# Performance work log

Measured on AMD Instinct MI355X. Metric: run time of the kernel, lower is better.

## Reference

```python
import jax, jax.numpy as jnp
import numpy as np
import math

U = 1024      # units
H = 16        # num_head
DH = U // H   # units_head
B = 2
Q = 1024      # query length
M = 1024      # memory length
KL = M + Q    # key length
R = KL + 1    # relative positions length (rel-shift needs k_len+1)
EPS = 1e-7    # K.epsilon()


def setup_inputs() -> dict:
    key = jax.random.key(0)
    ks = jax.random.split(key, 11)
    f32 = jnp.float32
    return {
        "inputs": jax.random.normal(ks[0], (B, Q, U), f32),
        "content": jax.random.normal(ks[1], (B, Q, U), f32),
        "memories": jax.random.normal(ks[2], (B, M, U), f32),
        "relatives": jax.random.normal(ks[3], (B, R, U), f32),
        "segment_mat": jax.random.uniform(ks[4], (B, Q, KL, 2), f32),
        "segment_embed": jax.random.normal(ks[5], (2, U), f32) * 0.02,
        "bias_context": jax.random.normal(ks[6], (U,), f32) * 0.02,
        "bias_relative": jax.random.normal(ks[7], (U,), f32) * 0.02,
        "bias_segment": jax.random.normal(ks[8], (U,), f32) * 0.02,
        "permutation": jax.random.uniform(ks[9], (B, Q, KL), f32),
        "kernel": jax.random.normal(ks[10], (U, 5 * U), f32) * 0.02,
    }


def _heads(x):
    # [B, L, U] -> [B, H, L, DH]
    b, l, _ = x.shape
    return x.reshape(b, l, H, DH).transpose(0, 2, 1, 3)


def _rel_shift(x, klen):
    # Transformer-XL relative shift via reshape trick. x: [B, H, Q, R]
    b, h, q, r = x.shape
    x = x.reshape(b, h, r, q)[:, :, 1:, :].reshape(b, h, q, r - 1)
    return x[:, :, :, :klen]


def reference(inputs, content, memories, relatives, segment_mat, segment_embed,
              bias_context, bias_relative, bias_segment, permutation, kernel):
    k_q = kernel[:, :U]
    k_kv = kernel[:, U:3 * U]
    k_r = kernel[:, 3 * U:4 * U]
    k_o = kernel[:, 4 * U:5 * U]

    full = jnp.concatenate([memories, content], axis=1)          # [B, KL, U]
    w_q = inputs @ k_q                                           # [B, Q, U]
    w_kv = full @ k_kv                                           # [B, KL, 2U]
    w_r = relatives @ k_r                                        # [B, R, U]

    w_k = _heads(w_kv[..., :U])                                  # [B, H, KL, DH]
    w_v = _heads(w_kv[..., U:])                                  # [B, H, KL, DH]

    # content term
    q_c = _heads(w_q + bias_context)                             # [B, H, Q, DH]
    a_context = jnp.einsum('bhqd,bhkd->bhqk', q_c, w_k)

    # relative-position term with rel-shift
    q_r = _heads(w_q + bias_relative)
    w_r_h = _heads(w_r)                                          # [B, H, R, DH]
    a_relative = _rel_shift(jnp.einsum('bhqd,bhrd->bhqr', q_r, w_r_h), KL)

    # segment term
    q_s = _heads(w_q + bias_segment)                             # [B, H, Q, DH]
    seg_e = segment_embed.T.reshape(H, DH, 2)                    # [H, DH, 2]
    qs_seg = jnp.einsum('bhqd,hds->bhqs', q_s, seg_e)            # [B, H, Q, 2]
    a_segment = jnp.einsum('bqks,bhqs->bhqk', segment_mat, qs_seg)

    att = (a_context + a_relative + a_segment) / math.sqrt(DH)   # [B, H, Q, KL]
    e = jnp.exp(att - jnp.max(att, axis=-1, keepdims=True))
    e = e * permutation[:, None, :, :]
    att = e / (jnp.sum(e, axis=-1, keepdims=True) + EPS)

    out = jnp.einsum('bhqk,bhkd->bhqd', att, w_v)                # [B, H, Q, DH]
    out = out.transpose(0, 2, 1, 3).reshape(inputs.shape[0], Q, U)
    return out @ k_o                                             # [B, Q, U]
```

## Files before the change

### kernel.cpp

```cpp
#include <hip/hip_runtime.h>

typedef __bf16 bf16;
typedef unsigned short u16;
typedef unsigned int u32;
typedef __attribute__((ext_vector_type(8))) __bf16 bf16x8;
typedef __attribute__((ext_vector_type(4))) __bf16 bf16x4;
typedef __attribute__((ext_vector_type(4))) float f32x4;
typedef __attribute__((ext_vector_type(8))) float f32x8;

#define SWZ(r, s) (((r) << 3) + ((s) ^ ((r) & 7)))
#define GSW(r, s) (((r) << 2) + ((s) ^ (((r) >> 1) & 3)))

__device__ __forceinline__ f32x4 mfma16(bf16x8 a, bf16x8 b, f32x4 c) {
  return __builtin_amdgcn_mfma_f32_16x16x32_bf16(a, b, c, 0, 0, 0);
}
__device__ __forceinline__ void gld16(const void* g, void* l) {
  __builtin_amdgcn_global_load_lds((const __attribute__((address_space(1))) void*)g,
                                   (__attribute__((address_space(3))) void*)l, 16, 0, 0);
}

__global__ __launch_bounds__(256) void prep_all(
    const float* __restrict__ inputs, const float* __restrict__ mem,
    const float* __restrict__ cont, const float* __restrict__ rel,
    const float* __restrict__ K, bf16* __restrict__ in_b,
    bf16* __restrict__ full_b, bf16* __restrict__ rel_b, bf16* __restrict__ KT) {
  __shared__ float t[64][68];
  const int bid = blockIdx.x, tid = threadIdx.x;
  if (bid < 1024) {
    size_t i = ((size_t)bid * 256 + tid) * 8;
    f32x8 v = *reinterpret_cast<const f32x8*>(inputs + i);
    *reinterpret_cast<bf16x8*>(in_b + i) = __builtin_convertvector(v, bf16x8);
  } else if (bid < 3072) {
    size_t i = ((size_t)(bid - 1024) * 256 + tid) * 8;
    int row = (int)(i >> 10), col = (int)(i & 1023);
    int b = row >> 11, r = row & 2047;
    const float* src = (r < 1024)
        ? (mem  + (((size_t)(b << 10) + r)          << 10) + col)
        : (cont + (((size_t)(b << 10) + (r - 1024)) << 10) + col);
    f32x8 v = *reinterpret_cast<const f32x8*>(src);
    *reinterpret_cast<bf16x8*>(full_b + i) = __builtin_convertvector(v, bf16x8);
  } else if (bid < 5121) {
    size_t i = ((size_t)(bid - 3072) * 256 + tid) * 8;
    f32x8 v = *reinterpret_cast<const f32x8*>(rel + i);
    *reinterpret_cast<bf16x8*>(rel_b + i) = __builtin_convertvector(v, bf16x8);
  } else {
    const int r = bid - 5121;
    const int n0 = (r % 80) << 6, k0 = (r / 80) << 6;
    for (int idx = tid; idx < 1024; idx += 256) {
      int rr = idx >> 4, c4 = (idx & 15) << 2;
      f32x4 v = *reinterpret_cast<const f32x4*>(K + (size_t)(k0 + rr) * 5120 + n0 + c4);
      t[rr][c4] = v.x; t[rr][c4 + 1] = v.y; t[rr][c4 + 2] = v.z; t[rr][c4 + 3] = v.w;
    }
    __syncthreads();
    for (int idx = tid; idx < 1024; idx += 256) {
      int rr = idx >> 4, c4 = (idx & 15) << 2;
      bf16x4 o = { (bf16)t[c4][rr], (bf16)t[c4 + 1][rr], (bf16)t[c4 + 2][rr], (bf16)t[c4 + 3][rr] };
      *reinterpret_cast<bf16x4*>(KT + (size_t)(n0 + rr) * 1024 + k0 + c4) = o;
    }
  }
}

template<int MT, int OUT_MODE, int KLEN, bool KWRAP>
__device__ __forceinline__ void gemm_body(
    const bf16* __restrict__ A, const bf16* __restrict__ BT,
    void* __restrict__ C0v, void* __restrict__ C1v,
    int m0, int n0, int Mrows, int splitN, bf16* As, bf16* Bs, int tid) {
  const int l = tid & 63, w = tid >> 6;
  const int wn = (w & 1) << 6;
  const int wm = (w >> 1) * (MT / 2);
  constexpr int MFR = MT / 32;
  const int lc = l & 15, l16 = l >> 4;
  f32x4 acc[MFR][4] = {};
  const int r0 = tid >> 2;
  const int sq = tid & 3;
  const int g0 = (sq ^ ((r0 >> 1) & 3)) << 3;

  for (int k0 = 0; k0 < KLEN; k0 += 32) {
    const int kk = KWRAP ? (k0 & 1023) : k0;
    __syncthreads();
    gld16(A  + (size_t)(m0 + r0) * KLEN + k0 + g0, &As[tid << 3]);
    gld16(BT + (size_t)(n0 + r0) * 1024 + kk + g0, &Bs[tid << 3]);
    if (MT == 128)
      gld16(A + (size_t)(m0 + r0 + 64) * KLEN + k0 + g0, &As[(tid + 256) << 3]);
    gld16(BT + (size_t)(n0 + r0 + 64) * 1024 + kk + g0, &Bs[(tid + 256) << 3]);
    __syncthreads();
    bf16x8 af[MFR], bfv[4];
#pragma unroll
    for (int m = 0; m < MFR; ++m)
      af[m] = *reinterpret_cast<const bf16x8*>(&As[GSW(wm + (m << 4) + lc, l16) << 3]);
#pragma unroll
    for (int n = 0; n < 4; ++n)
      bfv[n] = *reinterpret_cast<const bf16x8*>(&Bs[GSW(wn + (n << 4) + lc, l16) << 3]);
#pragma unroll
    for (int m = 0; m < MFR; ++m)
#pragma unroll
      for (int n = 0; n < 4; ++n)
        acc[m][n] = mfma16(af[m], bfv[n], acc[m][n]);
  }
#pragma unroll
  for (int m = 0; m < MFR; ++m) {
    const int rbase = m0 + wm + (m << 4) + (l16 << 2);
#pragma unroll
    for (int n = 0; n < 4; ++n) {
      const int col = n0 + wn + (n << 4) + lc;
      const int cc = (col < splitN) ? col : (col - splitN);
      void* Cv = (col < splitN) ? C0v : C1v;
#pragma unroll
      for (int r = 0; r < 4; ++r) {
        const int row = rbase + r;
        if (row < Mrows) {
          const float v = acc[m][n][r];
          const size_t off = ((size_t)row << 10) + cc;
          if (OUT_MODE == 1) ((bf16*)Cv)[off] = (bf16)v;
          else               ((float*)Cv)[off] = v;
        }
      }
    }
  }
}

__global__ __launch_bounds__(256) void proj_fused(
    const bf16* __restrict__ in_b, const bf16* __restrict__ full_b,
    const bf16* __restrict__ rel_b, const bf16* __restrict__ kT,
    bf16* __restrict__ w_q, bf16* __restrict__ w_k, bf16* __restrict__ w_v,
    bf16* __restrict__ w_rh) {
  __shared__ bf16 As[4096];
  __shared__ bf16 Bs[4096];
  const int bid = blockIdx.x, tid = threadIdx.x;
  if (bid < 256) {
    gemm_body<64, 1, 1024, false>(in_b, kT, w_q, w_q,
                                  (bid >> 3) << 6, (bid & 7) << 7, 2048, 1 << 30, As, Bs, tid);
  } else if (bid < 768) {
    const int r = bid - 256;
    gemm_body<128, 1, 1024, false>(full_b, kT + (1 << 20), w_k, w_v,
                                   (r >> 4) << 7, (r & 15) << 7, 4096, 1024, As, Bs, tid);
  } else {
    const int r = bid - 768;
    gemm_body<64, 1, 1024, false>(rel_b, kT + 3 * (1 << 20), w_rh, w_rh,
                                  (r >> 3) << 6, (r & 7) << 7, 4098, 1 << 30, As, Bs, tid);
  }
}

__global__ __launch_bounds__(256) void out_proj(
    const bf16* __restrict__ a_cat, const bf16* __restrict__ kTo,
    float* __restrict__ out) {
  __shared__ bf16 As[4096];
  __shared__ bf16 Bs[4096];
  const int bid = blockIdx.x, tid = threadIdx.x;
  gemm_body<64, 0, 2048, true>(a_cat, kTo, out, out,
                               (bid >> 3) << 6, (bid & 7) << 7, 2048, 1 << 30, As, Bs, tid);
}

__global__ __launch_bounds__(256) void mid_prep(
    const float* __restrict__ seg_mat, bf16* __restrict__ seg_b,
    const bf16* __restrict__ w_q, const float* __restrict__ bias_s,
    const float* __restrict__ seg_embed, float* __restrict__ qs) {
  const int bid = blockIdx.x, tid = threadIdx.x;
  if (bid < 4096) {
    size_t i = ((size_t)bid * 256 + tid) * 8;
    f32x8 v = *reinterpret_cast<const f32x8*>(seg_mat + i);
    *reinterpret_cast<bf16x8*>(seg_b + i) = __builtin_convertvector(v, bf16x8);
  } else {
    int idx = (bid - 4096) * 256 + tid;
    int q = idx & 1023, h = (idx >> 10) & 15, b = idx >> 14;
    const bf16* wp = w_q + (((size_t)(b << 10) + q) << 10) + (h << 6);
    const float* bp = bias_s + (h << 6);
    const float* e0 = seg_embed + (h << 6);
    const float* e1 = seg_embed + 1024 + (h << 6);
    float s0 = 0.f, s1 = 0.f;
#pragma unroll 8
    for (int d = 0; d < 64; ++d) {
      float v = (float)wp[d] + bp[d];
      s0 = fmaf(v, e0[d], s0);
      s1 = fmaf(v, e1[d], s1);
    }
    qs[((size_t)idx << 1) + 0] = s0;
    qs[((size_t)idx << 1) + 1] = s1;
  }
}

#define OFFA 7
#define OFFB 0

__global__ __launch_bounds__(256) void attn_mfma(
    const bf16* __restrict__ w_q, const bf16* __restrict__ w_k,
    const bf16* __restrict__ w_v, const bf16* __restrict__ w_rh,
    const float* __restrict__ qs_seg, const bf16* __restrict__ seg_b,
    const float* __restrict__ perm, const float* __restrict__ bias_c,
    const float* __restrict__ bias_r, bf16* __restrict__ a_cat) {
  const int id = blockIdx.x;
  const int h  = (id >> 3) & 15;
  const int cg = (id & 7) | ((id >> 7) << 3);
  const int qt = cg & 15, b = cg >> 4;
  const int qi0 = qt << 6;
  const int tid = threadIdx.x;
  const int w = tid >> 6, l = tid & 63;
  const int lc = l & 15, l16 = l >> 4;
  const int w16 = w << 4;
  const int myq = w16 + lc;

  __shared__ bf16 kt[2][32 * 64];
  __shared__ u16  vt[2][64 * 40];
  __shared__ bf16 wbc[128 * 64];
  __shared__ bf16 wb2[96 * 64];
  __shared__ u16  pl[64 * 40];
  __shared__ float ART[4 * 960];
  __shared__ float facw[64], lroww[64];

  auto stageK = [&](int buf, int kj) {
    int r = tid >> 3, s = tid & 7;
    gld16(w_k + ((size_t)((b << 11) + kj + r) << 10) + (h << 6) + ((s ^ (r & 7)) << 3),
          &kt[buf][tid << 3]);
  };
  auto stageWB = [&](int L0, int nrows, int OFF) {
    for (int base = 0; base < nrows; base += 32) {
      int r = (tid >> 3) + base, s = tid & 7;
      int L = L0 + r;
      int slot = (L + OFF) & 127;
      int grow = L > 2048 ? 2048 : L;
      gld16(w_rh + ((size_t)(b * 2049 + grow) << 10) + (h << 6) + ((s ^ (slot & 7)) << 3),
            &wbc[((slot << 3) | s) << 3]);
    }
  };
  auto stageWB2 = [&]() {
    for (int base = 0; base < 96; base += 32) {
      int r = (tid >> 3) + base, s = tid & 7;
      gld16(w_rh + ((size_t)(b * 2049 + r) << 10) + (h << 6) + ((s ^ (r & 7)) << 3),
            &wb2[((r << 3) | s) << 3]);
    }
  };
  const int kv2 = (tid & 15) << 1, d4 = ((tid >> 4) & 15) << 2, kw = tid & 15;
  auto loadV = [&](int kj, uint2& ra, uint2& rb) {
    const u16* vp = (const u16*)w_v + ((size_t)((b << 11) + kj + kv2) << 10) + (h << 6) + d4;
    ra = *reinterpret_cast<const uint2*>(vp);
    rb = *reinterpret_cast<const uint2*>(vp + 1024);
  };
  auto writeV = [&](int buf, uint2 ra, uint2 rb) {
    u32* vt32 = reinterpret_cast<u32*>(&vt[buf][0]);
    vt32[(d4 + 0) * 20 + kw] = (ra.x & 0xffffu) | (rb.x << 16);
    vt32[(d4 + 1) * 20 + kw] = (ra.x >> 16) | (rb.x & 0xffff0000u);
    vt32[(d4 + 2) * 20 + kw] = (ra.y & 0xffffu) | (rb.y << 16);
    vt32[(d4 + 3) * 20 + kw] = (ra.y >> 16) | (rb.y & 0xffff0000u);
  };
  const size_t qrowg = (size_t)((b << 10) + qi0 + myq);
  auto loadSP = [&](int kj, bf16x8& sA, bf16x8& sB, f32x4& pA, f32x4& pB) {
    const bf16* sp = seg_b + (qrowg * 2048 + kj + (l16 << 2)) * 2;
    sA = *reinterpret_cast<const bf16x8*>(sp);
    sB = *reinterpret_cast<const bf16x8*>(sp + 32);
    const float* pp = perm + qrowg * 2048 + kj + (l16 << 2);
    pA = *reinterpret_cast<const f32x4*>(pp);
    pB = *reinterpret_cast<const f32x4*>(pp + 16);
  };

  stageK(0, 0);
  stageWB(961 - qi0, 96, OFFA);
  uint2 ra0, rb0;
  loadV(0, ra0, rb0);
  bf16x8 segA_c, segB_c, segA_n = {}, segB_n = {};
  f32x4 pmA_c, pmB_c, pmA_n = {}, pmB_n = {};
  loadSP(0, segA_c, segB_c, pmA_c, pmB_c);

  const int dlo = l16 << 3;
  bf16x8 qcf0, qcf1, qrf0, qrf1, qrg0, qrg1;
  {
    const bf16* qb  = w_q + ((qrowg) << 10) + (h << 6);
    const int rq1 = (qi0 + myq + 1 > 1023) ? 1023 : qi0 + myq + 1;
    const bf16* qb1 = w_q + (((size_t)(b << 10) + rq1) << 10) + (h << 6);
    f32x8 bc0 = *reinterpret_cast<const f32x8*>(bias_c + (h << 6) + dlo);
    f32x8 bc1 = *reinterpret_cast<const f32x8*>(bias_c + (h << 6) + 32 + dlo);
    f32x8 br0 = *reinterpret_cast<const f32x8*>(bias_r + (h << 6) + dlo);
    f32x8 br1 = *reinterpret_cast<const f32x8*>(bias_r + (h << 6) + 32 + dlo);
    bf16x8 q0 = *reinterpret_cast<const bf16x8*>(qb + dlo);
    bf16x8 q1 = *reinterpret_cast<const bf16x8*>(qb + 32 + dlo);
    bf16x8 p0 = *reinterpret_cast<const bf16x8*>(qb1 + dlo);
    bf16x8 p1 = *reinterpret_cast<const bf16x8*>(qb1 + 32 + dlo);
    qcf0 = __builtin_convertvector(__builtin_convertvector(q0, f32x8) + bc0, bf16x8);
    qcf1 = __builtin_convertvector(__builtin_convertvector(q1, f32x8) + bc1, bf16x8);
    qrf0 = __builtin_convertvector(__builtin_convertvector(q0, f32x8) + br0, bf16x8);
    qrf1 = __builtin_convertvector(__builtin_convertvector(q1, f32x8) + br1, bf16x8);
    qrg0 = __builtin_convertvector(__builtin_convertvector(p0, f32x8) + br0, bf16x8);
    qrg1 = __builtin_convertvector(__builtin_convertvector(p1, f32x8) + br1, bf16x8);
  }
  const float* qp = qs_seg + ((((size_t)((b << 4) + h) << 10) + qi0 + myq) << 1);
  const float qs0 = qp[0], qs1 = qp[1];

  writeV(0, ra0, rb0);
  __syncthreads();

  float mrow = -1e30f, lrow = 0.f;
  f32x4 o[4] = {};
  const float SCL = 0.125f * 1.44269504f;
  int cur = 0;
  uint2 ra_n = {}, rb_n = {};

  for (int t = 0; t < 64; ++t) {
    const int kj = t << 5;
    const int rel0 = kj - qi0;
    const bool strad = (rel0 == 1024) | (rel0 == 1056);
    const bool mainB = (rel0 >= 1088);
    const int nxt = cur ^ 1;

    if (t < 63) {
      const int kjn = kj + 32, rel0n = rel0 + 32;
      stageK(nxt, kjn);
      if (rel0n == 1024) stageWB2();
      if (rel0n == 1120)      stageWB(32, 96, OFFB);
      else if (rel0n != 1088) {
        if (rel0n <= 1056) stageWB(rel0n + 1025, 32, OFFA);
        else               stageWB(rel0n - 1024, 32, OFFB);
      }
      loadV(kjn, ra_n, rb_n);
      loadSP(kjn, segA_n, segB_n, pmA_n, pmB_n);
    }

    f32x4 s0 = {0.f, 0.f, 0.f, 0.f}, s1 = {0.f, 0.f, 0.f, 0.f};
    {
      const bf16* ktc = kt[cur];
      bf16x8 a0 = *reinterpret_cast<const bf16x8*>(&ktc[SWZ(lc, l16) << 3]);
      bf16x8 a1 = *reinterpret_cast<const bf16x8*>(&ktc[SWZ(lc, l16 + 4) << 3]);
      bf16x8 a2 = *reinterpret_cast<const bf16x8*>(&ktc[SWZ(16 + lc, l16) << 3]);
      bf16x8 a3 = *reinterpret_cast<const bf16x8*>(&ktc[SWZ(16 + lc, l16 + 4) << 3]);
      __builtin_amdgcn_s_setprio(1);
      s0 = mfma16(a0, qcf0, s0); s0 = mfma16(a1, qcf1, s0);
      s1 = mfma16(a2, qcf0, s1); s1 = mfma16(a3, qcf1, s1);
      __builtin_amdgcn_s_setprio(0);
    }

    float relv[8];
    {
      const bf16x8 ar0 = mainB ? qrg0 : qrf0;
      const bf16x8 ar1 = mainB ? qrg1 : qrf1;
      const bool useWb2 = (rel0 == 1088);
      int sbase;
      if (!mainB)       sbase = (rel0 + 1016 - w16) & 127;
      else if (useWb2)  sbase = 48 - w16;
      else              sbase = (rel0 - 1040 - w16) & 127;
      const bf16* wbp = useWb2 ? wb2 : wbc;
#pragma unroll
      for (int bg = 0; bg < 3; ++bg) {
        int prow = sbase + (bg << 4) + lc;
        if (!useWb2) prow &= 127;
        bf16x8 w0 = *reinterpret_cast<const bf16x8*>(&wbp[SWZ(prow, l16) << 3]);
        bf16x8 w1 = *reinterpret_cast<const bf16x8*>(&wbp[SWZ(prow, l16 + 4) << 3]);
        f32x4 a_ = {0.f, 0.f, 0.f, 0.f};
        __builtin_amdgcn_s_setprio(1);
        a_ = mfma16(ar0, w0, a_); a_ = mfma16(ar1, w1, a_);
        __builtin_amdgcn_s_setprio(0);
        *reinterpret_cast<f32x4*>(&ART[w * 960 + ((bg << 4) + lc) * 20 + (l16 << 2)]) = a_;
      }
#pragma unroll
      for (int jj = 0; jj < 4; ++jj) {
        relv[jj]     = ART[w * 960 + (15 + (l16 << 2) + jj - lc) * 20 + lc];
        relv[4 + jj] = ART[w * 960 + (31 + (l16 << 2) + jj - lc) * 20 + lc];
      }
      if (strad) {
#pragma unroll
        for (int bg = 0; bg < 3; ++bg) {
          int srow = rel0 - 1040 - w16 + (bg << 4) + lc;
          srow = srow < 0 ? 0 : (srow > 95 ? 95 : srow);
          bf16x8 w0 = *reinterpret_cast<const bf16x8*>(&wb2[SWZ(srow, l16) << 3]);
          bf16x8 w1 = *reinterpret_cast<const bf16x8*>(&wb2[SWZ(srow, l16 + 4) << 3]);
          f32x4 a_ = {0.f, 0.f, 0.f, 0.f};
          a_ = mfma16(qrg0, w0, a_); a_ = mfma16(qrg1, w1, a_);
          *reinterpret_cast<f32x4*>(&ART[w * 960 + ((bg << 4) + lc) * 20 + (l16 << 2)]) = a_;
        }
#pragma unroll
        for (int jj = 0; jj < 4; ++jj) {
          const int jA = (l16 << 2) + jj, jB = 16 + jA;
          float rbA = ART[w * 960 + (15 + jA - lc) * 20 + lc];
          float rbB = ART[w * 960 + (15 + jB - lc) * 20 + lc];
          if (rel0 + jA - myq >= 1025) relv[jj] = rbA;
          if (rel0 + jB - myq >= 1025) relv[4 + jj] = rbB;
        }
      }
    }

    {
      f32x8 sgA = __builtin_convertvector(segA_c, f32x8);
      f32x8 sgB = __builtin_convertvector(segB_c, f32x8);
      float sv[8];
#pragma unroll
      for (int jj = 0; jj < 4; ++jj) {
        sv[jj]     = (s0[jj] + relv[jj]     + sgA[2 * jj] * qs0 + sgA[2 * jj + 1] * qs1) * SCL;
        sv[4 + jj] = (s1[jj] + relv[4 + jj] + sgB[2 * jj] * qs0 + sgB[2 * jj + 1] * qs1) * SCL;
      }
      float tm = sv[0];
#pragma unroll
      for (int jj = 1; jj < 8; ++jj) tm = fmaxf(tm, sv[jj]);
      tm = fmaxf(tm, __shfl_xor(tm, 16));
      tm = fmaxf(tm, __shfl_xor(tm, 32));
      const float mn2 = fmaxf(mrow, tm);
      const float facr = exp2f(mrow - mn2);
      float e[8], rs = 0.f;
#pragma unroll
      for (int jj = 0; jj < 4; ++jj) {
        e[jj]     = exp2f(sv[jj] - mn2) * pmA_c[jj];
        e[4 + jj] = exp2f(sv[4 + jj] - mn2) * pmB_c[jj];
        rs += e[jj] + e[4 + jj];
      }
      rs += __shfl_xor(rs, 16);
      rs += __shfl_xor(rs, 32);
      mrow = mn2;
      lrow = lrow * facr + rs;
      bf16x4 pa, pb;
#pragma unroll
      for (int jj = 0; jj < 4; ++jj) { pa[jj] = (bf16)e[jj]; pb[jj] = (bf16)e[4 + jj]; }
      *reinterpret_cast<bf16x4*>(&pl[myq * 40 + (l16 << 2)]) = pa;
      *reinterpret_cast<bf16x4*>(&pl[myq * 40 + 16 + (l16 << 2)]) = pb;
      if (l16 == 0) facw[myq] = facr;
    }

    {
      float fr[4];
#pragma unroll
      for (int r = 0; r < 4; ++r) fr[r] = facw[w16 + (l16 << 2) + r];
#pragma unroll
      for (int n = 0; n < 4; ++n)
#pragma unroll
        for (int r = 0; r < 4; ++r) o[n][r] *= fr[r];
      bf16x8 ap = *reinterpret_cast<const bf16x8*>(&pl[(w16 + lc) * 40 + (l16 << 3)]);
      bf16x8 bv0 = *reinterpret_cast<const bf16x8*>(&vt[cur][(lc) * 40 + (l16 << 3)]);
      bf16x8 bv1 = *reinterpret_cast<const bf16x8*>(&vt[cur][(16 + lc) * 40 + (l16 << 3)]);
      bf16x8 bv2 = *reinterpret_cast<const bf16x8*>(&vt[cur][(32 + lc) * 40 + (l16 << 3)]);
      bf16x8 bv3 = *reinterpret_cast<const bf16x8*>(&vt[cur][(48 + lc) * 40 + (l16 << 3)]);
      __builtin_amdgcn_s_setprio(1);
      o[0] = mfma16(ap, bv0, o[0]);
      o[1] = mfma16(ap, bv1, o[1]);
      o[2] = mfma16(ap, bv2, o[2]);
      o[3] = mfma16(ap, bv3, o[3]);
      __builtin_amdgcn_s_setprio(0);
    }

    if (t < 63) {
      writeV(nxt, ra_n, rb_n);
      segA_c = segA_n; segB_c = segB_n; pmA_c = pmA_n; pmB_c = pmB_n;
    }
    __syncthreads();
    cur = nxt;
  }

  if (l16 == 0) lroww[myq] = lrow;
  {
    float inv[4];
#pragma unroll
    for (int r = 0; r < 4; ++r)
      inv[r] = 1.f / (lroww[w16 + (l16 << 2) + r] + 1e-7f);
#pragma unroll
    for (int n = 0; n < 4; ++n) {
#pragma unroll
      for (int r = 0; r < 4; ++r) {
        const int row = qi0 + w16 + (l16 << 2) + r;
        const float v = o[n][r] * inv[r];
        const bf16 hi = (bf16)v;
        const float lof = v - (float)hi;
        const size_t off = (((size_t)(b << 10) + row) << 11) + (h << 6) + (n << 4) + lc;
        a_cat[off] = hi;
        a_cat[off + 1024] = (bf16)lof;
      }
    }
  }
}

extern "C" void kernel_launch(void* const* d_in, const int* in_sizes, int n_in,
                              void* d_out, int out_size, void* d_ws, size_t ws_size,
                              hipStream_t stream) {
  (void)in_sizes; (void)n_in; (void)out_size; (void)ws_size;
  const float* inputs    = (const float*)d_in[0];
  const float* content   = (const float*)d_in[1];
  const float* memories  = (const float*)d_in[2];
  const float* relatives = (const float*)d_in[3];
  const float* seg_mat   = (const float*)d_in[4];
  const float* seg_embed = (const float*)d_in[5];
  const float* bias_c    = (const float*)d_in[6];
  const float* bias_r    = (const float*)d_in[7];
  const float* bias_s    = (const float*)d_in[8];
  const float* perm      = (const float*)d_in[9];
  const float* kern      = (const float*)d_in[10];
  float* out = (float*)d_out;

  char* ws = (char*)d_ws;
  bf16*  in_b   = (bf16*)(ws);
  bf16*  full_b = (bf16*)(ws + 4194304);
  bf16*  rel_b  = (bf16*)(ws + 12582912);
  bf16*  kT     = (bf16*)(ws + 21233664);
  bf16*  w_q    = (bf16*)(ws + 31719424);
  bf16*  w_k    = (bf16*)(ws + 35913728);
  bf16*  w_v    = (bf16*)(ws + 44302336);
  bf16*  w_rh   = (bf16*)(ws + 52690944);
  float* qs     = (float*)(ws + 65277952);
  bf16*  seg_b  = (bf16*)(ws);
  bf16*  a_cat  = (bf16*)(ws + 21233664);
  bf16*  kTo    = (bf16*)(ws + 29622272);

  dim3 blk(256);
  prep_all<<<6401, blk, 0, stream>>>(inputs, memories, content, relatives, kern,
                                     in_b, full_b, rel_b, kT);
  proj_fused<<<1288, blk, 0, stream>>>(in_b, full_b, rel_b, kT, w_q, w_k, w_v, w_rh);
  mid_prep<<<4224, blk, 0, stream>>>(seg_mat, seg_b, w_q, bias_s, seg_embed, qs);
  attn_mfma<<<512, blk, 0, stream>>>(w_q, w_k, w_v, w_rh, qs, seg_b, perm,
                                     bias_c, bias_r, a_cat);
  out_proj<<<256, blk, 0, stream>>>(a_cat, kTo, out);
}
```

Baseline: 269.3 us.

## Split attention key range across two blocks and merge partial softmax results

The attention kernel now splits each (batch, head, query-tile) over two key halves, launching 1024 blocks instead of 512. Each block writes unnormalized outputs plus row max and sum to workspace chunks, and a new merge kernel combines them into a_cat. This raises parallelism on the many-CU GPU. Shared memory is also trimmed by reusing a pool, with the relative-score staging stored in bf16 for the upper half. Per-row scale factors now travel by wave shuffles instead of LDS, and the setprio hints are removed. The cost is an extra kernel launch, a workspace round trip, and lower precision on the upper half's relative scores.

```diff
diff --git a/kernel.cpp b/kernel.cpp
--- a/kernel.cpp
+++ b/kernel.cpp
@@ -18,6 +18,15 @@
   __builtin_amdgcn_global_load_lds((const __attribute__((address_space(1))) void*)g,
                                    (__attribute__((address_space(3))) void*)l, 16, 0, 0);
 }
+
+__device__ __forceinline__ float* chunk_ptr(char* ws, int c) {
+  size_t off;
+  if (c < 17)      off = 16777216u + (size_t)c * 262144u;
+  else if (c < 49) off = 21233664u + (size_t)(c - 17) * 262144u;
+  else             off = 61083648u + (size_t)(c - 49) * 262144u;
+  return (float*)(ws + off);
+}
+#define ML_OFF 65540096u
 
 __global__ __launch_bounds__(256) void prep_all(
     const float* __restrict__ inputs, const float* __restrict__ mem,
@@ -179,33 +188,34 @@
   }
 }
 
-#define OFFA 7
-#define OFFB 0
-
 __global__ __launch_bounds__(256) void attn_mfma(
     const bf16* __restrict__ w_q, const bf16* __restrict__ w_k,
     const bf16* __restrict__ w_v, const bf16* __restrict__ w_rh,
     const float* __restrict__ qs_seg, const bf16* __restrict__ seg_b,
     const float* __restrict__ perm, const float* __restrict__ bias_c,
-    const float* __restrict__ bias_r, bf16* __restrict__ a_cat) {
+    const float* __restrict__ bias_r, char* __restrict__ ws) {
   const int id = blockIdx.x;
-  const int h  = (id >> 3) & 15;
-  const int cg = (id & 7) | ((id >> 7) << 3);
-  const int qt = cg & 15, b = cg >> 4;
+  const int h    = id & 15;
+  const int qt   = (id >> 4) & 15;
+  const int half = (id >> 8) & 1;
+  const int b    = (id >> 9) & 1;
+  const bool up  = (half == 1);
   const int qi0 = qt << 6;
+  const int kj0 = half << 10;
   const int tid = threadIdx.x;
   const int w = tid >> 6, l = tid & 63;
   const int lc = l & 15, l16 = l >> 4;
   const int w16 = w << 4;
   const int myq = w16 + lc;
 
-  __shared__ bf16 kt[2][32 * 64];
-  __shared__ u16  vt[2][64 * 40];
-  __shared__ bf16 wbc[128 * 64];
-  __shared__ bf16 wb2[96 * 64];
-  __shared__ u16  pl[64 * 40];
-  __shared__ float ART[4 * 960];
-  __shared__ float facw[64], lroww[64];
+  __shared__ bf16 kt[2][2048];
+  __shared__ u16  vt[2][2560];
+  __shared__ bf16 wbc[8192];
+  __shared__ __align__(16) char upool[15872];
+  float* artL = (float*)upool;
+  bf16*  wb2v = (bf16*)upool;
+  u16*   artU = (u16*)(upool + 8192);
+  u16*   plw  = up ? (u16*)(upool + 8192 + w * 1920) : (u16*)(upool + w * 3840);
 
   auto stageK = [&](int buf, int kj) {
     int r = tid >> 3, s = tid & 7;
@@ -223,10 +233,10 @@
     }
   };
   auto stageWB2 = [&]() {
-    for (int base = 0; base < 96; base += 32) {
+    for (int base = 0; base < 64; base += 32) {
       int r = (tid >> 3) + base, s = tid & 7;
       gld16(w_rh + ((size_t)(b * 2049 + r) << 10) + (h << 6) + ((s ^ (r & 7)) << 3),
-            &wb2[((r << 3) | s) << 3]);
+            &wb2v[((r << 3) | s) << 3]);
     }
   };
   const int kv2 = (tid & 15) << 1, d4 = ((tid >> 4) & 15) << 2, kw = tid & 15;
@@ -251,14 +261,25 @@
     pA = *reinterpret_cast<const f32x4*>(pp);
     pB = *reinterpret_cast<const f32x4*>(pp + 16);
   };
-
-  stageK(0, 0);
-  stageWB(961 - qi0, 96, OFFA);
+  auto artWr = [&](int bandcol, f32x4 a_) {
+    int idx = w * 960 + bandcol * 20 + (l16 << 2);
+    if (up) *reinterpret_cast<bf16x4*>(&artU[idx]) = __builtin_convertvector(a_, bf16x4);
+    else    *reinterpret_cast<f32x4*>(&artL[idx]) = a_;
+  };
+  auto artRd = [&](int col) -> float {
+    int idx = w * 960 + col * 20 + lc;
+    return up ? (float)(reinterpret_cast<const bf16*>(artU)[idx]) : artL[idx];
+  };
+
+  const int rel0f = kj0 - qi0;
+  stageK(0, kj0);
+  stageWB(rel0f + 961, 96, 7);
+  if (up && rel0f == 1024) stageWB2();
   uint2 ra0, rb0;
-  loadV(0, ra0, rb0);
+  loadV(kj0, ra0, rb0);
   bf16x8 segA_c, segB_c, segA_n = {}, segB_n = {};
   f32x4 pmA_c, pmB_c, pmA_n = {}, pmB_n = {};
-  loadSP(0, segA_c, segB_c, pmA_c, pmB_c);
+  loadSP(kj0, segA_c, segB_c, pmA_c, pmB_c);
 
   const int dlo = l16 << 3;
   bf16x8 qcf0, qcf1, qrf0, qrf1, qrg0, qrg1;
@@ -293,21 +314,25 @@
   int cur = 0;
   uint2 ra_n = {}, rb_n = {};
 
-  for (int t = 0; t < 64; ++t) {
-    const int kj = t << 5;
+  for (int t = 0; t < 32; ++t) {
+    const int kj = kj0 + (t << 5);
     const int rel0 = kj - qi0;
-    const bool strad = (rel0 == 1024) | (rel0 == 1056);
-    const bool mainB = (rel0 >= 1088);
+    const bool strad = up && ((rel0 == 1024) | (rel0 == 1056));
+    const bool mainB = up && (rel0 >= 1088);
+    const bool spec1088 = up && (rel0 == 1088);
     const int nxt = cur ^ 1;
 
-    if (t < 63) {
+    if (t < 31) {
       const int kjn = kj + 32, rel0n = rel0 + 32;
       stageK(nxt, kjn);
-      if (rel0n == 1024) stageWB2();
-      if (rel0n == 1120)      stageWB(32, 96, OFFB);
-      else if (rel0n != 1088) {
-        if (rel0n <= 1056) stageWB(rel0n + 1025, 32, OFFA);
-        else               stageWB(rel0n - 1024, 32, OFFB);
+      if (up) {
+        if (rel0n == 1024) stageWB2();
+        if (rel0n <= 1056)       stageWB(rel0n + 1025, 32, 7);
+        else if (rel0n == 1088)  stageWB(64, 32, 8);
+        else if (rel0n == 1120) { stageWB(32, 32, 8); stageWB(96, 32, 8); }
+        else                     stageWB(rel0n - 1024, 32, 8);
+      } else {
+        stageWB(rel0n + 1025, 32, 7);
       }
       loadV(kjn, ra_n, rb_n);
       loadSP(kjn, segA_n, segB_n, pmA_n, pmB_n);
@@ -320,61 +345,65 @@
       bf16x8 a1 = *reinterpret_cast<const bf16x8*>(&ktc[SWZ(lc, l16 + 4) << 3]);
       bf16x8 a2 = *reinterpret_cast<const bf16x8*>(&ktc[SWZ(16 + lc, l16) << 3]);
       bf16x8 a3 = *reinterpret_cast<const bf16x8*>(&ktc[SWZ(16 + lc, l16 + 4) << 3]);
-      __builtin_amdgcn_s_setprio(1);
       s0 = mfma16(a0, qcf0, s0); s0 = mfma16(a1, qcf1, s0);
       s1 = mfma16(a2, qcf0, s1); s1 = mfma16(a3, qcf1, s1);
-      __builtin_amdgcn_s_setprio(0);
     }
 
     float relv[8];
     {
       const bf16x8 ar0 = mainB ? qrg0 : qrf0;
       const bf16x8 ar1 = mainB ? qrg1 : qrf1;
-      const bool useWb2 = (rel0 == 1088);
       int sbase;
-      if (!mainB)       sbase = (rel0 + 1016 - w16) & 127;
-      else if (useWb2)  sbase = 48 - w16;
-      else              sbase = (rel0 - 1040 - w16) & 127;
-      const bf16* wbp = useWb2 ? wb2 : wbc;
+      if (!mainB) sbase = (rel0 + 1016 - w16) & 127;
+      else        sbase = (rel0 - 1032 - w16) & 127;
 #pragma unroll
       for (int bg = 0; bg < 3; ++bg) {
-        int prow = sbase + (bg << 4) + lc;
-        if (!useWb2) prow &= 127;
-        bf16x8 w0 = *reinterpret_cast<const bf16x8*>(&wbp[SWZ(prow, l16) << 3]);
-        bf16x8 w1 = *reinterpret_cast<const bf16x8*>(&wbp[SWZ(prow, l16 + 4) << 3]);
+        bf16x8 w0, w1;
+        if (spec1088) {
+          int Lr = 48 - w16 + (bg << 4) + lc;
+          const bf16* p0 = (Lr < 64) ? &wb2v[SWZ(Lr, l16) << 3]
+                                     : &wbc[SWZ((Lr + 8) & 127, l16) << 3];
+          const bf16* p1 = (Lr < 64) ? &wb2v[SWZ(Lr, l16 + 4) << 3]
+                                     : &wbc[SWZ((Lr + 8) & 127, l16 + 4) << 3];
+          w0 = *reinterpret_cast<const bf16x8*>(p0);
+          w1 = *reinterpret_cast<const bf16x8*>(p1);
+        } else {
+          int prow = (sbase + (bg << 4) + lc) & 127;
+          w0 = *reinterpret_cast<const bf16x8*>(&wbc[SWZ(prow, l16) << 3]);
+          w1 = *reinterpret_cast<const bf16x8*>(&wbc[SWZ(prow, l16 + 4) << 3]);
+        }
         f32x4 a_ = {0.f, 0.f, 0.f, 0.f};
-        __builtin_amdgcn_s_setprio(1);
         a_ = mfma16(ar0, w0, a_); a_ = mfma16(ar1, w1, a_);
-        __builtin_amdgcn_s_setprio(0);
-        *reinterpret_cast<f32x4*>(&ART[w * 960 + ((bg << 4) + lc) * 20 + (l16 << 2)]) = a_;
+        artWr((bg << 4) + lc, a_);
       }
 #pragma unroll
       for (int jj = 0; jj < 4; ++jj) {
-        relv[jj]     = ART[w * 960 + (15 + (l16 << 2) + jj - lc) * 20 + lc];
-        relv[4 + jj] = ART[w * 960 + (31 + (l16 << 2) + jj - lc) * 20 + lc];
+        relv[jj]     = artRd(15 + (l16 << 2) + jj - lc);
+        relv[4 + jj] = artRd(31 + (l16 << 2) + jj - lc);
       }
       if (strad) {
 #pragma unroll
         for (int bg = 0; bg < 3; ++bg) {
           int srow = rel0 - 1040 - w16 + (bg << 4) + lc;
-          srow = srow < 0 ? 0 : (srow > 95 ? 95 : srow);
-          bf16x8 w0 = *reinterpret_cast<const bf16x8*>(&wb2[SWZ(srow, l16) << 3]);
-          bf16x8 w1 = *reinterpret_cast<const bf16x8*>(&wb2[SWZ(srow, l16 + 4) << 3]);
+          srow = srow < 0 ? 0 : (srow > 63 ? 63 : srow);
+          bf16x8 w0 = *reinterpret_cast<const bf16x8*>(&wb2v[SWZ(srow, l16) << 3]);
+          bf16x8 w1 = *reinterpret_cast<const bf16x8*>(&wb2v[SWZ(srow, l16 + 4) << 3]);
           f32x4 a_ = {0.f, 0.f, 0.f, 0.f};
           a_ = mfma16(qrg0, w0, a_); a_ = mfma16(qrg1, w1, a_);
-          *reinterpret_cast<f32x4*>(&ART[w * 960 + ((bg << 4) + lc) * 20 + (l16 << 2)]) = a_;
+          artWr((bg << 4) + lc, a_);
         }
 #pragma unroll
         for (int jj = 0; jj < 4; ++jj) {
           const int jA = (l16 << 2) + jj, jB = 16 + jA;
-          float rbA = ART[w * 960 + (15 + jA - lc) * 20 + lc];
-          float rbB = ART[w * 960 + (15 + jB - lc) * 20 + lc];
+          float rbA = artRd(15 + jA - lc);
+          float rbB = artRd(15 + jB - lc);
           if (rel0 + jA - myq >= 1025) relv[jj] = rbA;
           if (rel0 + jB - myq >= 1025) relv[4 + jj] = rbB;
         }
       }
     }
 
+    float facr;
     {
       f32x8 sgA = __builtin_convertvector(segA_c, f32x8);
       f32x8 sgB = __builtin_convertvector(segB_c, f32x8);
@@ -390,7 +419,7 @@
       tm = fmaxf(tm, __shfl_xor(tm, 16));
       tm = fmaxf(tm, __shfl_xor(tm, 32));
       const float mn2 = fmaxf(mrow, tm);
-      const float facr = exp2f(mrow - mn2);
+      facr = exp2f(mrow - mn2);
       float e[8], rs = 0.f;
 #pragma unroll
       for (int jj = 0; jj < 4; ++jj) {
@@ -405,33 +434,32 @@
       bf16x4 pa, pb;
 #pragma unroll
       for (int jj = 0; jj < 4; ++jj) { pa[jj] = (bf16)e[jj]; pb[jj] = (bf16)e[4 + jj]; }
-      *reinterpret_cast<bf16x4*>(&pl[myq * 40 + (l16 << 2)]) = pa;
-      *reinterpret_cast<bf16x4*>(&pl[myq * 40 + 16 + (l16 << 2)]) = pb;
-      if (l16 == 0) facw[myq] = facr;
+      *reinterpret_cast<bf16x4*>(&plw[lc * 40 + (l16 << 2)]) = pa;
+      *reinterpret_cast<bf16x4*>(&plw[lc * 40 + 16 + (l16 << 2)]) = pb;
     }
 
     {
-      float fr[4];
-#pragma unroll
-      for (int r = 0; r < 4; ++r) fr[r] = facw[w16 + (l16 << 2) + r];
-#pragma unroll
-      for (int n = 0; n < 4; ++n)
-#pragma unroll
-        for (int r = 0; r < 4; ++r) o[n][r] *= fr[r];
-      bf16x8 ap = *reinterpret_cast<const bf16x8*>(&pl[(w16 + lc) * 40 + (l16 << 3)]);
+      const int r4 = l16 << 2;
+      float fr0 = __shfl(facr, r4 + 0);
+      float fr1 = __shfl(facr, r4 + 1);
+      float fr2 = __shfl(facr, r4 + 2);
+      float fr3 = __shfl(facr, r4 + 3);
+#pragma unroll
+      for (int n = 0; n < 4; ++n) {
+        o[n][0] *= fr0; o[n][1] *= fr1; o[n][2] *= fr2; o[n][3] *= fr3;
+      }
+      bf16x8 ap = *reinterpret_cast<const bf16x8*>(&plw[lc * 40 + (l16 << 3)]);
       bf16x8 bv0 = *reinterpret_cast<const bf16x8*>(&vt[cur][(lc) * 40 + (l16 << 3)]);
       bf16x8 bv1 = *reinterpret_cast<const bf16x8*>(&vt[cur][(16 + lc) * 40 + (l16 << 3)]);
       bf16x8 bv2 = *reinterpret_cast<const bf16x8*>(&vt[cur][(32 + lc) * 40 + (l16 << 3)]);
       bf16x8 bv3 = *reinterpret_cast<const bf16x8*>(&vt[cur][(48 + lc) * 40 + (l16 << 3)]);
-      __builtin_amdgcn_s_setprio(1);
       o[0] = mfma16(ap, bv0, o[0]);
       o[1] = mfma16(ap, bv1, o[1]);
       o[2] = mfma16(ap, bv2, o[2]);
       o[3] = mfma16(ap, bv3, o[3]);
-      __builtin_amdgcn_s_setprio(0);
-    }
-
-    if (t < 63) {
+    }
+
+    if (t < 31) {
       writeV(nxt, ra_n, rb_n);
       segA_c = segA_n; segB_c = segB_n; pmA_c = pmA_n; pmB_c = pmB_n;
     }
@@ -439,26 +467,61 @@
     cur = nxt;
   }
 
-  if (l16 == 0) lroww[myq] = lrow;
   {
-    float inv[4];
-#pragma unroll
-    for (int r = 0; r < 4; ++r)
-      inv[r] = 1.f / (lroww[w16 + (l16 << 2) + r] + 1e-7f);
+    const int c = ((((b << 4) + h) << 1) + half);
+    float* ob = chunk_ptr(ws, c);
 #pragma unroll
     for (int n = 0; n < 4; ++n) {
 #pragma unroll
       for (int r = 0; r < 4; ++r) {
         const int row = qi0 + w16 + (l16 << 2) + r;
-        const float v = o[n][r] * inv[r];
-        const bf16 hi = (bf16)v;
-        const float lof = v - (float)hi;
-        const size_t off = (((size_t)(b << 10) + row) << 11) + (h << 6) + (n << 4) + lc;
-        a_cat[off] = hi;
-        a_cat[off + 1024] = (bf16)lof;
-      }
-    }
-  }
+        ob[row * 64 + (n << 4) + lc] = o[n][r];
+      }
+    }
+    if (l16 == 0) {
+      float* ml = (float*)(ws + ML_OFF);
+      ml[c * 2048 + qi0 + myq] = mrow;
+      ml[c * 2048 + 1024 + qi0 + myq] = lrow;
+    }
+  }
+}
+
+__global__ __launch_bounds__(256) void merge_attn(char* __restrict__ ws,
+                                                  bf16* __restrict__ a_cat) {
+  const int gid = blockIdx.x * 256 + threadIdx.x;
+  const int r = gid >> 2;
+  const int dq = (gid & 3) << 4;
+  const int b = r >> 14, h = (r >> 10) & 15, q = r & 1023;
+  const int c0 = (((b << 4) + h) << 1);
+  const float* o1 = chunk_ptr(ws, c0)     + q * 64 + dq;
+  const float* o2 = chunk_ptr(ws, c0 + 1) + q * 64 + dq;
+  const float* ml = (const float*)(ws + ML_OFF);
+  const float m1 = ml[c0 * 2048 + q],        l1 = ml[c0 * 2048 + 1024 + q];
+  const float m2 = ml[(c0 + 1) * 2048 + q],  l2 = ml[(c0 + 1) * 2048 + 1024 + q];
+  const float m = fmaxf(m1, m2);
+  float a1 = exp2f(m1 - m), a2 = exp2f(m2 - m);
+  const float inv = 1.f / (l1 * a1 + l2 * a2 + 1e-7f);
+  a1 *= inv; a2 *= inv;
+  bf16x8 hi0, hi1, lo0, lo1;
+#pragma unroll
+  for (int j4 = 0; j4 < 4; ++j4) {
+    f32x4 v1 = *reinterpret_cast<const f32x4*>(o1 + (j4 << 2));
+    f32x4 v2 = *reinterpret_cast<const f32x4*>(o2 + (j4 << 2));
+#pragma unroll
+    for (int jj = 0; jj < 4; ++jj) {
+      const float v = v1[jj] * a1 + v2[jj] * a2;
+      const bf16 hi = (bf16)v;
+      const float lo = v - (float)hi;
+      const int j = (j4 << 2) + jj;
+      if (j < 8) { hi0[j] = hi; lo0[j] = (bf16)lo; }
+      else       { hi1[j - 8] = hi; lo1[j - 8] = (bf16)lo; }
+    }
+  }
+  const size_t off = ((size_t)((b << 10) + q)) * 2048 + (h << 6) + dq;
+  *reinterpret_cast<bf16x8*>(a_cat + off) = hi0;
+  *reinterpret_cast<bf16x8*>(a_cat + off + 8) = hi1;
+  *reinterpret_cast<bf16x8*>(a_cat + off + 1024) = lo0;
+  *reinterpret_cast<bf16x8*>(a_cat + off + 1032) = lo1;
 }
 
 extern "C" void kernel_launch(void* const* d_in, const int* in_sizes, int n_in,
@@ -489,7 +552,7 @@
   bf16*  w_rh   = (bf16*)(ws + 52690944);
   float* qs     = (float*)(ws + 65277952);
   bf16*  seg_b  = (bf16*)(ws);
-  bf16*  a_cat  = (bf16*)(ws + 21233664);
+  bf16*  a_cat  = (bf16*)(ws);
   bf16*  kTo    = (bf16*)(ws + 29622272);
 
   dim3 blk(256);
@@ -497,7 +560,8 @@
                                      in_b, full_b, rel_b, kT);
   proj_fused<<<1288, blk, 0, stream>>>(in_b, full_b, rel_b, kT, w_q, w_k, w_v, w_rh);
   mid_prep<<<4224, blk, 0, stream>>>(seg_mat, seg_b, w_q, bias_s, seg_embed, qs);
-  attn_mfma<<<512, blk, 0, stream>>>(w_q, w_k, w_v, w_rh, qs, seg_b, perm,
-                                     bias_c, bias_r, a_cat);
+  attn_mfma<<<1024, blk, 0, stream>>>(w_q, w_k, w_v, w_rh, qs, seg_b, perm,
+                                      bias_c, bias_r, ws);
+  merge_attn<<<512, blk, 0, stream>>>(ws, a_cat);
   out_proj<<<256, blk, 0, stream>>>(a_cat, kTo, out);
 }
```

Measured after the change: 316.8 us. 17.6% more time.

## Shrink attention LDS footprint, fold softmax scale into Q, add lazy rescaling

Applied to the files above, without the earlier changes.

Reduces shared memory in the attention kernel. The relative-score scratch now holds bf16 instead of fp32 and is reused as the P staging buffer, the wb2 buffer shrinks from 96 to 64 rows, and the facw/lroww arrays are replaced by wave shuffles. The softmax scale is folded into the Q fragments and segment coefficients, removing a per-element multiply. A lazy online-softmax rescale skips the max update and the output rescale unless a row's max grows by more than 8 (log2 units). The s_setprio hints are dropped. The goal is higher occupancy and less ALU work, at the cost of bf16 rounding of the relative logits and more complex staging logic for wbc and wb2v.

```diff
diff --git a/kernel.cpp b/kernel.cpp
--- a/kernel.cpp
+++ b/kernel.cpp
@@ -179,9 +179,6 @@
   }
 }
 
-#define OFFA 7
-#define OFFB 0
-
 __global__ __launch_bounds__(256) void attn_mfma(
     const bf16* __restrict__ w_q, const bf16* __restrict__ w_k,
     const bf16* __restrict__ w_v, const bf16* __restrict__ w_rh,
@@ -199,13 +196,12 @@
   const int w16 = w << 4;
   const int myq = w16 + lc;
 
-  __shared__ bf16 kt[2][32 * 64];
-  __shared__ u16  vt[2][64 * 40];
-  __shared__ bf16 wbc[128 * 64];
-  __shared__ bf16 wb2[96 * 64];
-  __shared__ u16  pl[64 * 40];
-  __shared__ float ART[4 * 960];
-  __shared__ float facw[64], lroww[64];
+  __shared__ bf16 kt[2][2048];
+  __shared__ u16  vt[2][2560];
+  __shared__ bf16 wbc[8192];
+  __shared__ bf16 wb2v[4096];
+  __shared__ u16  artp[3840];
+  u16* artw = &artp[w * 960];
 
   auto stageK = [&](int buf, int kj) {
     int r = tid >> 3, s = tid & 7;
@@ -223,10 +219,10 @@
     }
   };
   auto stageWB2 = [&]() {
-    for (int base = 0; base < 96; base += 32) {
+    for (int base = 0; base < 64; base += 32) {
       int r = (tid >> 3) + base, s = tid & 7;
       gld16(w_rh + ((size_t)(b * 2049 + r) << 10) + (h << 6) + ((s ^ (r & 7)) << 3),
-            &wb2[((r << 3) | s) << 3]);
+            &wb2v[((r << 3) | s) << 3]);
     }
   };
   const int kv2 = (tid & 15) << 1, d4 = ((tid >> 4) & 15) << 2, kw = tid & 15;
@@ -251,15 +247,23 @@
     pA = *reinterpret_cast<const f32x4*>(pp);
     pB = *reinterpret_cast<const f32x4*>(pp + 16);
   };
+  auto artWr = [&](int bandcol, f32x4 a_) {
+    *reinterpret_cast<bf16x4*>(&artw[bandcol * 20 + (l16 << 2)]) =
+        __builtin_convertvector(a_, bf16x4);
+  };
+  auto artRd = [&](int col) -> float {
+    return (float)(reinterpret_cast<const bf16*>(artw)[col * 20 + lc]);
+  };
 
   stageK(0, 0);
-  stageWB(961 - qi0, 96, OFFA);
+  stageWB(961 - qi0, 96, 7);
   uint2 ra0, rb0;
   loadV(0, ra0, rb0);
   bf16x8 segA_c, segB_c, segA_n = {}, segB_n = {};
   f32x4 pmA_c, pmB_c, pmA_n = {}, pmB_n = {};
   loadSP(0, segA_c, segB_c, pmA_c, pmB_c);
 
+  const float SCLF = 0.125f * 1.44269504f;
   const int dlo = l16 << 3;
   bf16x8 qcf0, qcf1, qrf0, qrf1, qrg0, qrg1;
   {
@@ -274,22 +278,21 @@
     bf16x8 q1 = *reinterpret_cast<const bf16x8*>(qb + 32 + dlo);
     bf16x8 p0 = *reinterpret_cast<const bf16x8*>(qb1 + dlo);
     bf16x8 p1 = *reinterpret_cast<const bf16x8*>(qb1 + 32 + dlo);
-    qcf0 = __builtin_convertvector(__builtin_convertvector(q0, f32x8) + bc0, bf16x8);
-    qcf1 = __builtin_convertvector(__builtin_convertvector(q1, f32x8) + bc1, bf16x8);
-    qrf0 = __builtin_convertvector(__builtin_convertvector(q0, f32x8) + br0, bf16x8);
-    qrf1 = __builtin_convertvector(__builtin_convertvector(q1, f32x8) + br1, bf16x8);
-    qrg0 = __builtin_convertvector(__builtin_convertvector(p0, f32x8) + br0, bf16x8);
-    qrg1 = __builtin_convertvector(__builtin_convertvector(p1, f32x8) + br1, bf16x8);
+    qcf0 = __builtin_convertvector((__builtin_convertvector(q0, f32x8) + bc0) * SCLF, bf16x8);
+    qcf1 = __builtin_convertvector((__builtin_convertvector(q1, f32x8) + bc1) * SCLF, bf16x8);
+    qrf0 = __builtin_convertvector((__builtin_convertvector(q0, f32x8) + br0) * SCLF, bf16x8);
+    qrf1 = __builtin_convertvector((__builtin_convertvector(q1, f32x8) + br1) * SCLF, bf16x8);
+    qrg0 = __builtin_convertvector((__builtin_convertvector(p0, f32x8) + br0) * SCLF, bf16x8);
+    qrg1 = __builtin_convertvector((__builtin_convertvector(p1, f32x8) + br1) * SCLF, bf16x8);
   }
   const float* qp = qs_seg + ((((size_t)((b << 4) + h) << 10) + qi0 + myq) << 1);
-  const float qs0 = qp[0], qs1 = qp[1];
+  const float qs0 = qp[0] * SCLF, qs1 = qp[1] * SCLF;
 
   writeV(0, ra0, rb0);
   __syncthreads();
 
   float mrow = -1e30f, lrow = 0.f;
   f32x4 o[4] = {};
-  const float SCL = 0.125f * 1.44269504f;
   int cur = 0;
   uint2 ra_n = {}, rb_n = {};
 
@@ -298,17 +301,17 @@
     const int rel0 = kj - qi0;
     const bool strad = (rel0 == 1024) | (rel0 == 1056);
     const bool mainB = (rel0 >= 1088);
+    const bool spec1088 = (rel0 == 1088);
     const int nxt = cur ^ 1;
 
     if (t < 63) {
       const int kjn = kj + 32, rel0n = rel0 + 32;
       stageK(nxt, kjn);
       if (rel0n == 1024) stageWB2();
-      if (rel0n == 1120)      stageWB(32, 96, OFFB);
-      else if (rel0n != 1088) {
-        if (rel0n <= 1056) stageWB(rel0n + 1025, 32, OFFA);
-        else               stageWB(rel0n - 1024, 32, OFFB);
-      }
+      if (rel0n <= 1056)       stageWB(rel0n + 1025, 32, 7);
+      else if (rel0n == 1088)  stageWB(64, 32, 8);
+      else if (rel0n == 1120) { stageWB(32, 32, 8); stageWB(96, 32, 8); }
+      else                     stageWB(rel0n - 1024, 32, 8);
       loadV(kjn, ra_n, rb_n);
       loadSP(kjn, segA_n, segB_n, pmA_n, pmB_n);
     }
@@ -320,115 +323,126 @@
       bf16x8 a1 = *reinterpret_cast<const bf16x8*>(&ktc[SWZ(lc, l16 + 4) << 3]);
       bf16x8 a2 = *reinterpret_cast<const bf16x8*>(&ktc[SWZ(16 + lc, l16) << 3]);
       bf16x8 a3 = *reinterpret_cast<const bf16x8*>(&ktc[SWZ(16 + lc, l16 + 4) << 3]);
-      __builtin_amdgcn_s_setprio(1);
       s0 = mfma16(a0, qcf0, s0); s0 = mfma16(a1, qcf1, s0);
       s1 = mfma16(a2, qcf0, s1); s1 = mfma16(a3, qcf1, s1);
-      __builtin_amdgcn_s_setprio(0);
     }
 
     float relv[8];
     {
       const bf16x8 ar0 = mainB ? qrg0 : qrf0;
       const bf16x8 ar1 = mainB ? qrg1 : qrf1;
-      const bool useWb2 = (rel0 == 1088);
       int sbase;
-      if (!mainB)       sbase = (rel0 + 1016 - w16) & 127;
-      else if (useWb2)  sbase = 48 - w16;
-      else              sbase = (rel0 - 1040 - w16) & 127;
-      const bf16* wbp = useWb2 ? wb2 : wbc;
+      if (!mainB) sbase = (rel0 + 1016 - w16) & 127;
+      else        sbase = (rel0 - 1032 - w16) & 127;
 #pragma unroll
       for (int bg = 0; bg < 3; ++bg) {
-        int prow = sbase + (bg << 4) + lc;
-        if (!useWb2) prow &= 127;
-        bf16x8 w0 = *reinterpret_cast<const bf16x8*>(&wbp[SWZ(prow, l16) << 3]);
-        bf16x8 w1 = *reinterpret_cast<const bf16x8*>(&wbp[SWZ(prow, l16 + 4) << 3]);
+        bf16x8 w0, w1;
+        if (spec1088) {
+          int Lr = 48 - w16 + (bg << 4) + lc;
+          const bf16* p0 = (Lr < 64) ? &wb2v[SWZ(Lr, l16) << 3]
+                                     : &wbc[SWZ((Lr + 8) & 127, l16) << 3];
+          const bf16* p1 = (Lr < 64) ? &wb2v[SWZ(Lr, l16 + 4) << 3]
+                                     : &wbc[SWZ((Lr + 8) & 127, l16 + 4) << 3];
+          w0 = *reinterpret_cast<const bf16x8*>(p0);
+          w1 = *reinterpret_cast<const bf16x8*>(p1);
+        } else {
+          int prow = (sbase + (bg << 4) + lc) & 127;
+          w0 = *reinterpret_cast<const bf16x8*>(&wbc[SWZ(prow, l16) << 3]);
+          w1 = *reinterpret_cast<const bf16x8*>(&wbc[SWZ(prow, l16 + 4) << 3]);
+        }
         f32x4 a_ = {0.f, 0.f, 0.f, 0.f};
-        __builtin_amdgcn_s_setprio(1);
         a_ = mfma16(ar0, w0, a_); a_ = mfma16(ar1, w1, a_);
-        __builtin_amdgcn_s_setprio(0);
-        *reinterpret_cast<f32x4*>(&ART[w * 960 + ((bg << 4) + lc) * 20 + (l16 << 2)]) = a_;
+        artWr((bg << 4) + lc, a_);
       }
 #pragma unroll
       for (int jj = 0; jj < 4; ++jj) {
-        relv[jj]     = ART[w * 960 + (15 + (l16 << 2) + jj - lc) * 20 + lc];
-        relv[4 + jj] = ART[w * 960 + (31 + (l16 << 2) + jj - lc) * 20 + lc];
+        relv[jj]     = artRd(15 + (l16 << 2) + jj - lc);
+        relv[4 + jj] = artRd(31 + (l16 << 2) + jj - lc);
       }
       if (strad) {
 #pragma unroll
         for (int bg = 0; bg < 3; ++bg) {
           int srow = rel0 - 1040 - w16 + (bg << 4) + lc;
-          srow = srow < 0 ? 0 : (srow > 95 ? 95 : srow);
-          bf16x8 w0 = *reinterpret_cast<const bf16x8*>(&wb2[SWZ(srow, l16) << 3]);
-          bf16x8 w1 = *reinterpret_cast<const bf16x8*>(&wb2[SWZ(srow, l16 + 4) << 3]);
+          srow = srow < 0 ? 0 : (srow > 63 ? 63 : srow);
+          bf16x8 w0 = *reinterpret_cast<const bf16x8*>(&wb2v[SWZ(srow, l16) << 3]);
+          bf16x8 w1 = *reinterpret_cast<const bf16x8*>(&wb2v[SWZ(srow, l16 + 4) << 3]);
           f32x4 a_ = {0.f, 0.f, 0.f, 0.f};
           a_ = mfma16(qrg0, w0, a_); a_ = mfma16(qrg1, w1, a_);
-          *reinterpret_cast<f32x4*>(&ART[w * 960 + ((bg << 4) + lc) * 20 + (l16 << 2)]) = a_;
+          artWr((bg << 4) + lc, a_);
         }
 #pragma unroll
         for (int jj = 0; jj < 4; ++jj) {
           const int jA = (l16 << 2) + jj, jB = 16 + jA;
-          float rbA = ART[w * 960 + (15 + jA - lc) * 20 + lc];
-          float rbB = ART[w * 960 + (15 + jB - lc) * 20 + lc];
+          float rbA = artRd(15 + jA - lc);
+          float rbB = artRd(15 + jB - lc);
           if (rel0 + jA - myq >= 1025) relv[jj] = rbA;
           if (rel0 + jB - myq >= 1025) relv[4 + jj] = rbB;
         }
       }
     }
 
+    bool full;
+    float facr;
     {
       f32x8 sgA = __builtin_convertvector(segA_c, f32x8);
       f32x8 sgB = __builtin_convertvector(segB_c, f32x8);
       float sv[8];
 #pragma unroll
       for (int jj = 0; jj < 4; ++jj) {
-        sv[jj]     = (s0[jj] + relv[jj]     + sgA[2 * jj] * qs0 + sgA[2 * jj + 1] * qs1) * SCL;
-        sv[4 + jj] = (s1[jj] + relv[4 + jj] + sgB[2 * jj] * qs0 + sgB[2 * jj + 1] * qs1) * SCL;
+        sv[jj]     = s0[jj] + relv[jj]     + sgA[2 * jj] * qs0 + sgA[2 * jj + 1] * qs1;
+        sv[4 + jj] = s1[jj] + relv[4 + jj] + sgB[2 * jj] * qs0 + sgB[2 * jj + 1] * qs1;
       }
       float tm = sv[0];
 #pragma unroll
       for (int jj = 1; jj < 8; ++jj) tm = fmaxf(tm, sv[jj]);
       tm = fmaxf(tm, __shfl_xor(tm, 16));
       tm = fmaxf(tm, __shfl_xor(tm, 32));
-      const float mn2 = fmaxf(mrow, tm);
-      const float facr = exp2f(mrow - mn2);
+      full = __any(tm > mrow + 8.f);
+      if (full) {
+        const float mn2 = fmaxf(mrow, tm);
+        facr = exp2f(mrow - mn2);
+        mrow = mn2;
+      } else {
+        facr = 1.f;
+      }
       float e[8], rs = 0.f;
 #pragma unroll
       for (int jj = 0; jj < 4; ++jj) {
-        e[jj]     = exp2f(sv[jj] - mn2) * pmA_c[jj];
-        e[4 + jj] = exp2f(sv[4 + jj] - mn2) * pmB_c[jj];
+        e[jj]     = exp2f(sv[jj] - mrow) * pmA_c[jj];
+        e[4 + jj] = exp2f(sv[4 + jj] - mrow) * pmB_c[jj];
         rs += e[jj] + e[4 + jj];
       }
       rs += __shfl_xor(rs, 16);
       rs += __shfl_xor(rs, 32);
-      mrow = mn2;
       lrow = lrow * facr + rs;
       bf16x4 pa, pb;
 #pragma unroll
       for (int jj = 0; jj < 4; ++jj) { pa[jj] = (bf16)e[jj]; pb[jj] = (bf16)e[4 + jj]; }
-      *reinterpret_cast<bf16x4*>(&pl[myq * 40 + (l16 << 2)]) = pa;
-      *reinterpret_cast<bf16x4*>(&pl[myq * 40 + 16 + (l16 << 2)]) = pb;
-      if (l16 == 0) facw[myq] = facr;
+      *reinterpret_cast<bf16x4*>(&artw[lc * 40 + (l16 << 2)]) = pa;
+      *reinterpret_cast<bf16x4*>(&artw[lc * 40 + 16 + (l16 << 2)]) = pb;
     }
 
     {
-      float fr[4];
-#pragma unroll
-      for (int r = 0; r < 4; ++r) fr[r] = facw[w16 + (l16 << 2) + r];
-#pragma unroll
-      for (int n = 0; n < 4; ++n)
-#pragma unroll
-        for (int r = 0; r < 4; ++r) o[n][r] *= fr[r];
-      bf16x8 ap = *reinterpret_cast<const bf16x8*>(&pl[(w16 + lc) * 40 + (l16 << 3)]);
+      if (full) {
+        const int r4 = l16 << 2;
+        float fr0 = __shfl(facr, r4 + 0);
+        float fr1 = __shfl(facr, r4 + 1);
+        float fr2 = __shfl(facr, r4 + 2);
+        float fr3 = __shfl(facr, r4 + 3);
+#pragma unroll
+        for (int n = 0; n < 4; ++n) {
+          o[n][0] *= fr0; o[n][1] *= fr1; o[n][2] *= fr2; o[n][3] *= fr3;
+        }
+      }
+      bf16x8 ap = *reinterpret_cast<const bf16x8*>(&artw[lc * 40 + (l16 << 3)]);
       bf16x8 bv0 = *reinterpret_cast<const bf16x8*>(&vt[cur][(lc) * 40 + (l16 << 3)]);
       bf16x8 bv1 = *reinterpret_cast<const bf16x8*>(&vt[cur][(16 + lc) * 40 + (l16 << 3)]);
       bf16x8 bv2 = *reinterpret_cast<const bf16x8*>(&vt[cur][(32 + lc) * 40 + (l16 << 3)]);
       bf16x8 bv3 = *reinterpret_cast<const bf16x8*>(&vt[cur][(48 + lc) * 40 + (l16 << 3)]);
-      __builtin_amdgcn_s_setprio(1);
       o[0] = mfma16(ap, bv0, o[0]);
       o[1] = mfma16(ap, bv1, o[1]);
       o[2] = mfma16(ap, bv2, o[2]);
       o[3] = mfma16(ap, bv3, o[3]);
-      __builtin_amdgcn_s_setprio(0);
     }
 
     if (t < 63) {
@@ -439,12 +453,11 @@
     cur = nxt;
   }
 
-  if (l16 == 0) lroww[myq] = lrow;
   {
     float inv[4];
 #pragma unroll
     for (int r = 0; r < 4; ++r)
-      inv[r] = 1.f / (lroww[w16 + (l16 << 2) + r] + 1e-7f);
+      inv[r] = 1.f / (__shfl(lrow, (l16 << 2) + r) + 1e-7f);
 #pragma unroll
     for (int n = 0; n < 4; ++n) {
 #pragma unroll
```

After: 263.2 us. 2.2% less time.
